# Optimization experiments

Measured on AMD Instinct MI355X. Metric: run time of the kernel, lower is better.

Reference implementation:

```python
import jax, jax.numpy as jnp
import numpy as np

N = 512            # input_size == number of graph nodes (X = I_N)
B = 64             # batch_size
H1, H2, H3 = 128, 64, 32   # hidden3 + 16 must equal 32 + class_nums
OUT = 8            # output_size; OUT*OUT + OUT == 72 (controller out channels)
CLS = 16           # class_nums (one-hot task encoding is 16-dim)


def setup_inputs():
    key = jax.random.key(0)
    ks = jax.random.split(key, 20)

    def u(k, shape, fan_out):
        s = 1.0 / np.sqrt(fan_out)
        return jax.random.uniform(k, shape, jnp.float32, -s, s)

    inp = {
        "adj": jax.random.uniform(ks[0], (B, 2, N, N), jnp.float32),
        "task_id": jax.random.randint(ks[1], (B,), 0, CLS),
    }
    dims = [(N, H1), (H1, H2), (H2, H3), (H3, OUT)]
    i = 2
    for pref in ("p", "n"):
        for l, (fi, fo) in enumerate(dims, 1):
            inp[f"w{l}{pref}"] = u(ks[i], (fi, fo), fo); i += 1
            inp[f"b{l}{pref}"] = u(ks[i], (fo,), fo); i += 1
    # controller: Conv1d(H3+CLS, 72, kernel=1, bias=False) -> stored as [72, H3+CLS]
    inp["wc"] = jax.random.normal(ks[i], (OUT * OUT + OUT, H3 + CLS), jnp.float32) * np.sqrt(2.0 / (OUT * OUT + OUT))
    return inp


def _normalize(adj):
    # D^-1/2 (A + I) D^-1/2, fully vectorized over [B, 2] (original loops in Python)
    a = adj + jnp.eye(adj.shape[-1], dtype=adj.dtype)
    d = a.sum(-1) ** -0.5                       # [B,2,N]
    return d[..., :, None] * a * d[..., None, :]


def _leaky(x):
    return jnp.where(x >= 0, x, 0.2 * x)


def _gcn_branch(feat, ws, bs):
    # feat: [B,N,N] normalized adjacency; X = I_N so first support = W1
    x = jnp.eye(N, dtype=feat.dtype)
    for i, (w, b) in enumerate(zip(ws, bs)):
        x = jnp.matmul(feat, jnp.matmul(x, w)) + b   # [B,N,fo]
        if i < len(ws) - 1:
            x = _leaky(x)
        if i == len(ws) - 2:
            conv3 = x
    return conv3, x                                  # ([B,N,H3], [B,N,OUT])


def _dcl(conv3, task_enc, conv4, wc):
    # conv3: [B,N,H3]; conv4: [B,N,OUT]; task_enc: [B,CLS]
    x_feat = conv3.mean(axis=1)                       # AdaptiveAvgPool1d over nodes -> [B,H3]
    x_cond = jnp.concatenate([x_feat, task_enc], 1)   # [B,H3+CLS]
    params = x_cond @ wc.T                            # [B,72]
    w = params[:, :OUT * OUT].reshape(B, OUT, OUT)    # per-sample dynamic head weights
    b = params[:, OUT * OUT:]                         # [B,OUT]
    # head_inputs = conv4.view(1,-1,N) with groups=B grouped conv1d (kernel 1)
    head = conv4.reshape(B, OUT, N)
    logits = jnp.einsum('boi,bin->bon', w, head) + b[..., None]   # [B,OUT,N]
    return logits.reshape(B, N, OUT)                  # faithful to torch reshape(N_,H_,-1)


def _forward(adj, task_id, w1p, b1p, w2p, b2p, w3p, b3p, w4p, b4p,
             w1n, b1n, w2n, b2n, w3n, b3n, w4n, b4n, wc):
    adj_n = _normalize(adj)
    feat_p, feat_n = adj_n[:, 0], adj_n[:, 1]
    p3, p4 = _gcn_branch(feat_p, [w1p, w2p, w3p, w4p], [b1p, b2p, b3p, b4p])
    n3, n4 = _gcn_branch(feat_n, [w1n, w2n, w3n, w4n], [b1n, b2n, b3n, b4n])
    te = jax.nn.one_hot(task_id, CLS, dtype=adj.dtype)   # encoding_task
    lp = _dcl(p3, te, p4, wc)
    ln = _dcl(n3, te, n4, wc)
    cc = jnp.concatenate([lp, ln], -1).reshape(-1, 2, N, OUT)  # [B,2,N,OUT]
    # F.dropout treated as identity (eval-mode determinism for reference)
    xm = jnp.matmul(cc, jnp.swapaxes(cc, -1, -2))              # [B,2,N,N]
    return jax.nn.log_sigmoid(xm) * -1.0


def reference(adj, task_id, w1p, b1p, w2p, b2p, w3p, b3p, w4p, b4p,
              w1n, b1n, w2n, b2n, w3n, b3n, w4n, b4n, wc):
    return _forward(adj, task_id, w1p, b1p, w2p, b2p, w3p, b3p, w4p, b4p,
                    w1n, b1n, w2n, b2n, w3n, b3n, w4n, b4n, wc)
```

## Files before the change

kernel.cpp:

```cpp
#include <hip/hip_runtime.h>
#include <math.h>

#define NN 512
#define NBC 128

__global__ __launch_bounds__(256) void k_rowsum(const float* __restrict__ adj,
                                                float* __restrict__ dinv) {
    int wave = blockIdx.x * 4 + (threadIdx.x >> 6);
    int lane = threadIdx.x & 63;
    const float4* row = (const float4*)(adj + (size_t)wave * NN);
    float4 v0 = row[lane], v1 = row[lane + 64];
    float s = v0.x + v0.y + v0.z + v0.w + v1.x + v1.y + v1.z + v1.w;
    #pragma unroll
    for (int off = 32; off; off >>= 1) s += __shfl_down(s, off, 64);
    if (lane == 0) dinv[wave] = rsqrtf(1.0f + s);
}

template<int H, int HP, bool SHARED, bool ACT>
__global__ __launch_bounds__(256) void k_biggemm(
    const float* __restrict__ adj, const float* __restrict__ zcg,
    const float* __restrict__ wp, const float* __restrict__ wn,
    const float* __restrict__ bp, const float* __restrict__ bn,
    const float* __restrict__ dinv, float* __restrict__ xout)
{
    constexpr int CPT = HP / 16;
    constexpr int KT = 64;
    __shared__ float a_s[64 * 68];
    __shared__ float z_s[KT * H];
    const int bc = blockIdx.y;
    const int rt = blockIdx.x;
    const int t  = threadIdx.x;
    const int tx = t & 15, ty = t >> 4;
    const float* A    = adj + (size_t)bc * NN * NN + (size_t)rt * 64 * NN;
    const float* dloc = dinv + bc * NN;
    const float* ZG   = SHARED ? ((bc & 1) ? wn : wp) : (zcg + (size_t)bc * NN * H);
    const float* bias = (bc & 1) ? bn : bp;

    float acc[4][CPT];
    #pragma unroll
    for (int r = 0; r < 4; ++r)
        #pragma unroll
        for (int u = 0; u < CPT; ++u) acc[r][u] = 0.f;

    for (int kb = 0; kb < NN; kb += KT) {
        __syncthreads();
        #pragma unroll
        for (int l = 0; l < 4; ++l) {
            int idx = t + l * 256;
            int r = idx >> 4, q = idx & 15;
            float4 v = *(const float4*)(A + (size_t)r * NN + kb + q * 4);
            *(float4*)(a_s + r * 68 + q * 4) = v;
        }
        constexpr int NZ4 = KT * H / 4;
        for (int idx = t; idx < NZ4; idx += 256) {
            int k = idx / (H / 4), hq = idx % (H / 4);
            float4 v = *(const float4*)(ZG + (size_t)(kb + k) * H + hq * 4);
            if (SHARED) {
                float dk = dloc[kb + k];
                v.x *= dk; v.y *= dk; v.z *= dk; v.w *= dk;
            }
            *(float4*)(z_s + k * H + hq * 4) = v;
        }
        __syncthreads();
        #pragma unroll 8
        for (int k = 0; k < KT; ++k) {
            float ar[4];
            #pragma unroll
            for (int r = 0; r < 4; ++r) ar[r] = a_s[(ty * 4 + r) * 68 + k];
            float zv[CPT];
            #pragma unroll
            for (int u = 0; u < CPT; ++u) {
                int h = tx * CPT + u;
                if (H < HP && h >= H) h = 0;
                zv[u] = z_s[k * H + h];
            }
            #pragma unroll
            for (int r = 0; r < 4; ++r)
                #pragma unroll
                for (int u = 0; u < CPT; ++u)
                    acc[r][u] += ar[r] * zv[u];
        }
    }
    #pragma unroll
    for (int r = 0; r < 4; ++r) {
        int i = rt * 64 + ty * 4 + r;
        float di = dloc[i];
        #pragma unroll
        for (int u = 0; u < CPT; ++u) {
            int h = tx * CPT + u;
            if (H < HP && h >= H) continue;
            float self = SHARED ? di * ZG[(size_t)i * H + h] : ZG[(size_t)i * H + h];
            float v = di * (acc[r][u] + self) + bias[h];
            if (ACT) v = v >= 0.f ? v : 0.2f * v;
            xout[((size_t)bc * NN + i) * H + h] = v;
        }
    }
}

template<int HI, int HO>
__global__ __launch_bounds__(256) void k_smallgemm(
    const float* __restrict__ xin, const float* __restrict__ wp,
    const float* __restrict__ wn, const float* __restrict__ dinv,
    float* __restrict__ zc)
{
    constexpr int CPT = (HO >= 16) ? HO / 16 : 1;
    constexpr int XS = HI + 4;
    __shared__ float x_s[32 * XS];
    __shared__ float w_s[HI * HO];
    const int bc = blockIdx.y, jt = blockIdx.x, t = threadIdx.x;
    const int tx = t & 15, ty = t >> 4;
    const float* W = (bc & 1) ? wn : wp;
    const float* X = xin + ((size_t)bc * NN + jt * 32) * HI;
    for (int idx = t; idx < HI * HO / 4; idx += 256)
        *(float4*)(w_s + idx * 4) = *(const float4*)(W + idx * 4);
    for (int idx = t; idx < 32 * HI / 4; idx += 256) {
        int r = idx / (HI / 4), q = idx % (HI / 4);
        *(float4*)(x_s + r * XS + q * 4) = *(const float4*)(X + (size_t)r * HI + q * 4);
    }
    __syncthreads();
    float acc[2][CPT];
    #pragma unroll
    for (int r = 0; r < 2; ++r)
        #pragma unroll
        for (int u = 0; u < CPT; ++u) acc[r][u] = 0.f;
    #pragma unroll 4
    for (int p = 0; p < HI; ++p) {
        float xr[2];
        #pragma unroll
        for (int r = 0; r < 2; ++r) xr[r] = x_s[(ty * 2 + r) * XS + p];
        float wv[CPT];
        #pragma unroll
        for (int u = 0; u < CPT; ++u) {
            int h = tx * CPT + u;
            if (HO < 16 && h >= HO) h = 0;
            wv[u] = w_s[p * HO + h];
        }
        #pragma unroll
        for (int r = 0; r < 2; ++r)
            #pragma unroll
            for (int u = 0; u < CPT; ++u) acc[r][u] += xr[r] * wv[u];
    }
    const float* dloc = dinv + bc * NN;
    #pragma unroll
    for (int r = 0; r < 2; ++r) {
        int j = jt * 32 + ty * 2 + r;
        float dj = dloc[j];
        #pragma unroll
        for (int u = 0; u < CPT; ++u) {
            int h = tx * CPT + u;
            if (HO < 16 && h >= HO) continue;
            zc[((size_t)bc * NN + j) * HO + h] = dj * acc[r][u];
        }
    }
}

__global__ __launch_bounds__(256) void k_dcl(
    const float* __restrict__ x3, const float* __restrict__ x4,
    const float* __restrict__ wc, const int* __restrict__ task,
    float* __restrict__ L)
{
    __shared__ float ps[8][32];
    __shared__ float xf[32];
    __shared__ float pr[72];
    const int bc = blockIdx.x, t = threadIdx.x;
    const float* X3 = x3 + (size_t)bc * NN * 32;
    {
        int col = t & 31, rg = t >> 5;
        float s = 0.f;
        for (int r = rg; r < NN; r += 8) s += X3[r * 32 + col];
        ps[rg][col] = s;
    }
    __syncthreads();
    if (t < 32) {
        float s = 0.f;
        #pragma unroll
        for (int g = 0; g < 8; ++g) s += ps[g][t];
        xf[t] = s * (1.0f / 512.0f);
    }
    __syncthreads();
    if (t < 72) {
        int tid = task[bc >> 1];
        const float* wr = wc + t * 48;
        float s = wr[32 + tid];
        #pragma unroll
        for (int j = 0; j < 32; ++j) s += wr[j] * xf[j];
        pr[t] = s;
    }
    __syncthreads();
    const float* X4 = x4 + (size_t)bc * 4096;
    float* Lb = L + (size_t)bc * 4096;
    #pragma unroll
    for (int rep = 0; rep < 2; ++rep) {
        int n = rep * 256 + t;
        float hi[8];
        #pragma unroll
        for (int i = 0; i < 8; ++i) hi[i] = X4[i * 512 + n];
        #pragma unroll
        for (int o = 0; o < 8; ++o) {
            float s = pr[64 + o];
            #pragma unroll
            for (int i = 0; i < 8; ++i) s += pr[o * 8 + i] * hi[i];
            Lb[o * 512 + n] = s;
        }
    }
}

#define SCP 520
__global__ __launch_bounds__(256) void k_final(const float* __restrict__ L,
                                               float* __restrict__ out)
{
    __shared__ float scT[8 * SCP];
    const int bcid = blockIdx.y;
    const int b = bcid >> 1, c = bcid & 1;
    const int nt = blockIdx.x, t = threadIdx.x;
    const float* Lp = L + (size_t)(b * 2) * 4096;
    const float* Ln = Lp + 4096;
    for (int rep = 0; rep < 16; ++rep) {
        int e = rep * 256 + t;
        int f = c * 4096 + e;
        int n = f >> 4, k = f & 15;
        float v = (k < 8) ? Lp[n * 8 + k] : Ln[n * 8 + k - 8];
        scT[(e & 7) * SCP + (e >> 3)] = v;
    }
    __syncthreads();
    const int tx = t & 63, ty = t >> 6;
    const int n0 = nt * 32 + ty * 8;
    float cn[8][8];
    #pragma unroll
    for (int o = 0; o < 8; ++o)
        #pragma unroll
        for (int i = 0; i < 8; ++i) cn[i][o] = scT[o * SCP + n0 + i];
    float* ob = out + (size_t)bcid * NN * NN;
    #pragma unroll 2
    for (int mg = 0; mg < 8; ++mg) {
        int m = tx + mg * 64;
        float cm[8];
        #pragma unroll
        for (int o = 0; o < 8; ++o) cm[o] = scT[o * SCP + m];
        #pragma unroll
        for (int i = 0; i < 8; ++i) {
            float s = 0.f;
            #pragma unroll
            for (int o = 0; o < 8; ++o) s += cn[i][o] * cm[o];
            float r = fmaxf(-s, 0.f) + __logf(1.0f + __expf(-fabsf(s)));
            ob[(size_t)(n0 + i) * NN + m] = r;
        }
    }
}

extern "C" void kernel_launch(void* const* d_in, const int* in_sizes, int n_in,
                              void* d_out, int out_size, void* d_ws, size_t ws_size,
                              hipStream_t stream)
{
    const float* adj = (const float*)d_in[0];
    const int*  task = (const int*)d_in[1];
    const float* w1p = (const float*)d_in[2];  const float* b1p = (const float*)d_in[3];
    const float* w2p = (const float*)d_in[4];  const float* b2p = (const float*)d_in[5];
    const float* w3p = (const float*)d_in[6];  const float* b3p = (const float*)d_in[7];
    const float* w4p = (const float*)d_in[8];  const float* b4p = (const float*)d_in[9];
    const float* w1n = (const float*)d_in[10]; const float* b1n = (const float*)d_in[11];
    const float* w2n = (const float*)d_in[12]; const float* b2n = (const float*)d_in[13];
    const float* w3n = (const float*)d_in[14]; const float* b3n = (const float*)d_in[15];
    const float* w4n = (const float*)d_in[16]; const float* b4n = (const float*)d_in[17];
    const float* wc  = (const float*)d_in[18];

    float* ws   = (float*)d_ws;
    float* dinv = ws;
    float* XA   = ws + 65536;
    float* X3   = XA + 8388608;
    float* X4   = X3 + 2097152;
    float* L    = X4 + 524288;
    float* ZC   = L  + 524288;
    (void)in_sizes; (void)n_in; (void)out_size; (void)ws_size;

    k_rowsum<<<dim3(NBC * NN / 4), dim3(256), 0, stream>>>(adj, dinv);
    k_biggemm<128,128,true ,true ><<<dim3(8,128), 256, 0, stream>>>(adj, nullptr, w1p, w1n, b1p, b1n, dinv, XA);
    k_smallgemm<128,64><<<dim3(16,128), 256, 0, stream>>>(XA, w2p, w2n, dinv, ZC);
    k_biggemm<64,64,false,true ><<<dim3(8,128), 256, 0, stream>>>(adj, ZC, nullptr, nullptr, b2p, b2n, dinv, XA);
    k_smallgemm<64,32><<<dim3(16,128), 256, 0, stream>>>(XA, w3p, w3n, dinv, ZC);
    k_biggemm<32,32,false,true ><<<dim3(8,128), 256, 0, stream>>>(adj, ZC, nullptr, nullptr, b3p, b3n, dinv, X3);
    k_smallgemm<32,8><<<dim3(16,128), 256, 0, stream>>>(X3, w4p, w4n, dinv, ZC);
    k_biggemm<8,16,false,false><<<dim3(8,128), 256, 0, stream>>>(adj, ZC, nullptr, nullptr, b4p, b4n, dinv, X4);
    k_dcl<<<dim3(128), 256, 0, stream>>>(X3, X4, wc, task, L);
    k_final<<<dim3(16,128), 256, 0, stream>>>(L, (float*)d_out);
}
```

Measured before the change: 617.0 us.

## Use split-bf16 MFMA GEMMs with a pre-normalized bf16 adjacency copy

Adds a path that normalizes the adjacency once and stores it as hi/lo bf16 pairs. All GCN GEMMs then run on MFMA 16x16x32 bf16 instructions, using three products per tile to keep close to fp32 accuracy. Weights are pre-transposed and split, and intermediate activations are written in split-bf16 form for the next layer. This trades extra memory traffic (a 128 MB adjacency copy plus conversion passes) and a ~198 MB workspace requirement for much higher matrix throughput than the scalar fp32 FMA kernels. The old path is kept as a fallback when the workspace is too small.

```diff
diff --git a/kernel.cpp b/kernel.cpp
--- a/kernel.cpp
+++ b/kernel.cpp
@@ -3,6 +3,19 @@
 
 #define NN 512
 #define NBC 128
+
+typedef __attribute__((ext_vector_type(8))) __bf16 v8bf;
+typedef __attribute__((ext_vector_type(4))) float v4f;
+
+__device__ __forceinline__ void bsplit(float v, unsigned short& h, unsigned short& l) {
+    unsigned u  = __builtin_bit_cast(unsigned, v);
+    unsigned hb = (u + 0x7fffu + ((u >> 16) & 1u)) & 0xffff0000u;
+    float hf    = __builtin_bit_cast(float, hb);
+    h = (unsigned short)(hb >> 16);
+    float lof   = v - hf;
+    unsigned ul = __builtin_bit_cast(unsigned, lof);
+    l = (unsigned short)((ul + 0x7fffu + ((ul >> 16) & 1u)) >> 16);
+}
 
 __global__ __launch_bounds__(256) void k_rowsum(const float* __restrict__ adj,
                                                 float* __restrict__ dinv) {
@@ -14,6 +27,153 @@
     #pragma unroll
     for (int off = 32; off; off >>= 1) s += __shfl_down(s, off, 64);
     if (lane == 0) dinv[wave] = rsqrtf(1.0f + s);
+}
+
+__global__ __launch_bounds__(256) void k_convert(const float* __restrict__ adj,
+    const float* __restrict__ dinv, unsigned short* __restrict__ anh,
+    unsigned short* __restrict__ anl)
+{
+    unsigned gid = blockIdx.x * 256 + threadIdx.x;
+    unsigned e = gid * 4;
+    unsigned bc = e >> 18, rem = e & 0x3ffffu;
+    unsigned i = rem >> 9, j = rem & 511u;
+    float4 a = *(const float4*)(adj + (size_t)e);
+    float di = dinv[bc * NN + i];
+    const float4 dj = *(const float4*)(dinv + bc * NN + j);
+    float v0 = di * dj.x * (a.x + ((j + 0) == i ? 1.f : 0.f));
+    float v1 = di * dj.y * (a.y + ((j + 1) == i ? 1.f : 0.f));
+    float v2 = di * dj.z * (a.z + ((j + 2) == i ? 1.f : 0.f));
+    float v3 = di * dj.w * (a.w + ((j + 3) == i ? 1.f : 0.f));
+    ushort4 hh, ll;
+    bsplit(v0, hh.x, ll.x); bsplit(v1, hh.y, ll.y);
+    bsplit(v2, hh.z, ll.z); bsplit(v3, hh.w, ll.w);
+    *(ushort4*)(anh + e) = hh;
+    *(ushort4*)(anl + e) = ll;
+}
+
+struct WJob  { const float* w; unsigned short* dh; unsigned short* dl; int HI; int HO; int HOP; };
+struct WJobs { WJob j[8]; };
+__global__ __launch_bounds__(256) void k_wprep(WJobs jobs) {
+    WJob jb = jobs.j[blockIdx.y];
+    int idx = blockIdx.x * 256 + threadIdx.x;
+    if (idx >= jb.HOP * jb.HI) return;
+    int h = idx / jb.HI, p = idx % jb.HI;
+    float v = (h < jb.HO) ? jb.w[p * jb.HO + h] : 0.f;
+    unsigned short hh, ll; bsplit(v, hh, ll);
+    jb.dh[idx] = hh; jb.dl[idx] = ll;
+}
+
+template<int BN, int OUTW, bool SHAREDZ, bool ACT, bool WBF>
+__global__ __launch_bounds__(256, 2) void k_mfma(
+    const unsigned short* __restrict__ anh_, const unsigned short* __restrict__ anl_,
+    const unsigned short* __restrict__ zh_,  const unsigned short* __restrict__ zl_,
+    const float* __restrict__ bp, const float* __restrict__ bn,
+    float* __restrict__ xf, unsigned short* __restrict__ xh, unsigned short* __restrict__ xl)
+{
+    constexpr int C = BN / 16;
+    const int bc = blockIdx.y, rb = blockIdx.x;
+    const int t = threadIdx.x, w = t >> 6, lane = t & 63;
+    const int m0 = lane & 15, quad = lane >> 4;
+    const int rowbase = rb * 128 + w * 32;
+    const int s = SHAREDZ ? (bc & 1) : bc;
+    const unsigned short* pa_h = anh_ + ((size_t)bc * NN + rowbase + m0) * NN + quad * 8;
+    const unsigned short* pa_l = anl_ + ((size_t)bc * NN + rowbase + m0) * NN + quad * 8;
+    const unsigned short* pz_h = zh_ + ((size_t)s * BN + m0) * NN + quad * 8;
+    const unsigned short* pz_l = zl_ + ((size_t)s * BN + m0) * NN + quad * 8;
+    v4f acc[2][C];
+    #pragma unroll
+    for (int r = 0; r < 2; ++r)
+        #pragma unroll
+        for (int c = 0; c < C; ++c) acc[r][c] = (v4f){0.f, 0.f, 0.f, 0.f};
+
+    for (int kb = 0; kb < 16; ++kb) {
+        const int ko = kb * 32;
+        v8bf zfh[C], zfl[C];
+        #pragma unroll
+        for (int c = 0; c < C; ++c) {
+            zfh[c] = *(const v8bf*)(pz_h + (size_t)(c * 16) * NN + ko);
+            zfl[c] = *(const v8bf*)(pz_l + (size_t)(c * 16) * NN + ko);
+        }
+        #pragma unroll
+        for (int r = 0; r < 2; ++r) {
+            v8bf ah = *(const v8bf*)(pa_h + (size_t)(r * 16) * NN + ko);
+            v8bf al = *(const v8bf*)(pa_l + (size_t)(r * 16) * NN + ko);
+            #pragma unroll
+            for (int c = 0; c < C; ++c) {
+                acc[r][c] = __builtin_amdgcn_mfma_f32_16x16x32_bf16(ah, zfh[c], acc[r][c], 0, 0, 0);
+                acc[r][c] = __builtin_amdgcn_mfma_f32_16x16x32_bf16(ah, zfl[c], acc[r][c], 0, 0, 0);
+                acc[r][c] = __builtin_amdgcn_mfma_f32_16x16x32_bf16(al, zfh[c], acc[r][c], 0, 0, 0);
+            }
+        }
+    }
+    const float* bias = (bc & 1) ? bn : bp;
+    #pragma unroll
+    for (int r = 0; r < 2; ++r)
+        #pragma unroll
+        for (int c = 0; c < C; ++c) {
+            int col = c * 16 + m0;
+            if (OUTW < BN && col >= OUTW) continue;
+            float bv = bias[col];
+            #pragma unroll
+            for (int reg = 0; reg < 4; ++reg) {
+                int row = rowbase + r * 16 + quad * 4 + reg;
+                float v = acc[r][c][reg] + bv;
+                if (ACT) v = v >= 0.f ? v : 0.2f * v;
+                size_t oi = ((size_t)bc * NN + row) * OUTW + col;
+                if (xf) xf[oi] = v;
+                if (WBF) {
+                    unsigned short hh, ll; bsplit(v, hh, ll);
+                    xh[oi] = hh; xl[oi] = ll;
+                }
+            }
+        }
+}
+
+template<int HI, int HOP>
+__global__ __launch_bounds__(256) void k_zgemm(
+    const unsigned short* __restrict__ wth, const unsigned short* __restrict__ wtl,
+    const unsigned short* __restrict__ xh_, const unsigned short* __restrict__ xl_,
+    unsigned short* __restrict__ zh_, unsigned short* __restrict__ zl_)
+{
+    constexpr int MT = HOP / 16, JW = 4 / MT, NT = 8 / JW;
+    const int bc = blockIdx.y, jb = blockIdx.x;
+    const int t = threadIdx.x, w = t >> 6, lane = t & 63;
+    const int m0 = lane & 15, quad = lane >> 4;
+    const int mt = w % MT, jseg = w / MT;
+    const int n0 = jb * 128 + jseg * (128 / JW);
+    const int s = bc & 1;
+    const unsigned short* pw_h = wth + ((size_t)s * HOP + mt * 16 + m0) * HI + quad * 8;
+    const unsigned short* pw_l = wtl + ((size_t)s * HOP + mt * 16 + m0) * HI + quad * 8;
+    const unsigned short* px_h = xh_ + ((size_t)bc * NN + n0 + m0) * HI + quad * 8;
+    const unsigned short* px_l = xl_ + ((size_t)bc * NN + n0 + m0) * HI + quad * 8;
+    v4f acc[NT];
+    #pragma unroll
+    for (int c = 0; c < NT; ++c) acc[c] = (v4f){0.f, 0.f, 0.f, 0.f};
+    #pragma unroll
+    for (int ks = 0; ks < HI / 32; ++ks) {
+        const int ko = ks * 32;
+        v8bf awh = *(const v8bf*)(pw_h + ko);
+        v8bf awl = *(const v8bf*)(pw_l + ko);
+        #pragma unroll
+        for (int c = 0; c < NT; ++c) {
+            v8bf bxh = *(const v8bf*)(px_h + (size_t)(c * 16) * HI + ko);
+            v8bf bxl = *(const v8bf*)(px_l + (size_t)(c * 16) * HI + ko);
+            acc[c] = __builtin_amdgcn_mfma_f32_16x16x32_bf16(awh, bxh, acc[c], 0, 0, 0);
+            acc[c] = __builtin_amdgcn_mfma_f32_16x16x32_bf16(awh, bxl, acc[c], 0, 0, 0);
+            acc[c] = __builtin_amdgcn_mfma_f32_16x16x32_bf16(awl, bxh, acc[c], 0, 0, 0);
+        }
+    }
+    #pragma unroll
+    for (int c = 0; c < NT; ++c) {
+        int j = n0 + c * 16 + m0;
+        #pragma unroll
+        for (int reg = 0; reg < 4; ++reg) {
+            int h = mt * 16 + quad * 4 + reg;
+            unsigned short hh, ll; bsplit(acc[c][reg], hh, ll);
+            size_t oi = ((size_t)bc * HOP + h) * NN + j;
+            zh_[oi] = hh; zl_[oi] = ll;
+        }
+    }
 }
 
 template<int H, int HP, bool SHARED, bool ACT>
@@ -35,13 +195,11 @@
     const float* dloc = dinv + bc * NN;
     const float* ZG   = SHARED ? ((bc & 1) ? wn : wp) : (zcg + (size_t)bc * NN * H);
     const float* bias = (bc & 1) ? bn : bp;
-
     float acc[4][CPT];
     #pragma unroll
     for (int r = 0; r < 4; ++r)
         #pragma unroll
         for (int u = 0; u < CPT; ++u) acc[r][u] = 0.f;
-
     for (int kb = 0; kb < NN; kb += KT) {
         __syncthreads();
         #pragma unroll
@@ -263,24 +421,77 @@
     const float* w3n = (const float*)d_in[14]; const float* b3n = (const float*)d_in[15];
     const float* w4n = (const float*)d_in[16]; const float* b4n = (const float*)d_in[17];
     const float* wc  = (const float*)d_in[18];
-
-    float* ws   = (float*)d_ws;
-    float* dinv = ws;
-    float* XA   = ws + 65536;
-    float* X3   = XA + 8388608;
-    float* X4   = X3 + 2097152;
-    float* L    = X4 + 524288;
-    float* ZC   = L  + 524288;
-    (void)in_sizes; (void)n_in; (void)out_size; (void)ws_size;
-
-    k_rowsum<<<dim3(NBC * NN / 4), dim3(256), 0, stream>>>(adj, dinv);
-    k_biggemm<128,128,true ,true ><<<dim3(8,128), 256, 0, stream>>>(adj, nullptr, w1p, w1n, b1p, b1n, dinv, XA);
-    k_smallgemm<128,64><<<dim3(16,128), 256, 0, stream>>>(XA, w2p, w2n, dinv, ZC);
-    k_biggemm<64,64,false,true ><<<dim3(8,128), 256, 0, stream>>>(adj, ZC, nullptr, nullptr, b2p, b2n, dinv, XA);
-    k_smallgemm<64,32><<<dim3(16,128), 256, 0, stream>>>(XA, w3p, w3n, dinv, ZC);
-    k_biggemm<32,32,false,true ><<<dim3(8,128), 256, 0, stream>>>(adj, ZC, nullptr, nullptr, b3p, b3n, dinv, X3);
-    k_smallgemm<32,8><<<dim3(16,128), 256, 0, stream>>>(X3, w4p, w4n, dinv, ZC);
-    k_biggemm<8,16,false,false><<<dim3(8,128), 256, 0, stream>>>(adj, ZC, nullptr, nullptr, b4p, b4n, dinv, X4);
-    k_dcl<<<dim3(128), 256, 0, stream>>>(X3, X4, wc, task, L);
-    k_final<<<dim3(16,128), 256, 0, stream>>>(L, (float*)d_out);
-}
+    (void)in_sizes; (void)n_in; (void)out_size;
+
+    const size_t NEED = 198004736ull;
+    if (ws_size >= NEED) {
+        char* base = (char*)d_ws;
+        float*          dinv = (float*)(base + 0);
+        unsigned short* anh  = (unsigned short*)(base + 262144);
+        unsigned short* anl  = (unsigned short*)(base + 67371008);
+        unsigned short* zt1h = (unsigned short*)(base + 134479872);
+        unsigned short* zt1l = (unsigned short*)(base + 134742016);
+        unsigned short* wt2h = (unsigned short*)(base + 135004160);
+        unsigned short* wt2l = (unsigned short*)(base + 135036928);
+        unsigned short* wt3h = (unsigned short*)(base + 135069696);
+        unsigned short* wt3l = (unsigned short*)(base + 135077888);
+        unsigned short* wt4h = (unsigned short*)(base + 135086080);
+        unsigned short* wt4l = (unsigned short*)(base + 135088128);
+        unsigned short* x1h  = (unsigned short*)(base + 135090176);
+        unsigned short* x1l  = (unsigned short*)(base + 151867392);
+        unsigned short* zt2h = (unsigned short*)(base + 168644608);
+        unsigned short* zt2l = (unsigned short*)(base + 177033216);
+        float*          x3f  = (float*)(base + 185421824);
+        float*          x4f  = (float*)(base + 193810432);
+        float*          L    = (float*)(base + 195907584);
+        unsigned short* x2h = x1h,  *x2l = x1l;
+        unsigned short* x3h = x1h,  *x3l = x1l;
+        unsigned short* zt3h = zt2h, *zt3l = zt2l;
+        unsigned short* zt4h = zt2h, *zt4l = zt2l;
+
+        k_rowsum<<<dim3(NBC * NN / 4), 256, 0, stream>>>(adj, dinv);
+        k_convert<<<dim3(32768), 256, 0, stream>>>(adj, dinv, anh, anl);
+        WJobs jobs;
+        jobs.j[0] = {w1p, zt1h,          zt1l,          512, 128, 128};
+        jobs.j[1] = {w1n, zt1h + 65536,  zt1l + 65536,  512, 128, 128};
+        jobs.j[2] = {w2p, wt2h,          wt2l,          128,  64,  64};
+        jobs.j[3] = {w2n, wt2h + 8192,   wt2l + 8192,   128,  64,  64};
+        jobs.j[4] = {w3p, wt3h,          wt3l,           64,  32,  32};
+        jobs.j[5] = {w3n, wt3h + 2048,   wt3l + 2048,    64,  32,  32};
+        jobs.j[6] = {w4p, wt4h,          wt4l,           32,   8,  16};
+        jobs.j[7] = {w4n, wt4h + 512,    wt4l + 512,     32,   8,  16};
+        k_wprep<<<dim3(256, 8), 256, 0, stream>>>(jobs);
+
+        k_mfma<128, 128, true,  true,  true ><<<dim3(4, NBC), 256, 0, stream>>>(
+            anh, anl, zt1h, zt1l, b1p, b1n, nullptr, x1h, x1l);
+        k_zgemm<128, 64><<<dim3(4, NBC), 256, 0, stream>>>(wt2h, wt2l, x1h, x1l, zt2h, zt2l);
+        k_mfma<64, 64, false, true,  true ><<<dim3(4, NBC), 256, 0, stream>>>(
+            anh, anl, zt2h, zt2l, b2p, b2n, nullptr, x2h, x2l);
+        k_zgemm<64, 32><<<dim3(4, NBC), 256, 0, stream>>>(wt3h, wt3l, x2h, x2l, zt3h, zt3l);
+        k_mfma<32, 32, false, true,  true ><<<dim3(4, NBC), 256, 0, stream>>>(
+            anh, anl, zt3h, zt3l, b3p, b3n, x3f, x3h, x3l);
+        k_zgemm<32, 16><<<dim3(4, NBC), 256, 0, stream>>>(wt4h, wt4l, x3h, x3l, zt4h, zt4l);
+        k_mfma<16, 8, false, false, false><<<dim3(4, NBC), 256, 0, stream>>>(
+            anh, anl, zt4h, zt4l, b4p, b4n, x4f, nullptr, nullptr);
+        k_dcl<<<dim3(NBC), 256, 0, stream>>>(x3f, x4f, wc, task, L);
+        k_final<<<dim3(16, NBC), 256, 0, stream>>>(L, (float*)d_out);
+    } else {
+        float* ws   = (float*)d_ws;
+        float* dinv = ws;
+        float* XA   = ws + 65536;
+        float* X3   = XA + 8388608;
+        float* X4   = X3 + 2097152;
+        float* L    = X4 + 524288;
+        float* ZC   = L  + 524288;
+        k_rowsum<<<dim3(NBC * NN / 4), 256, 0, stream>>>(adj, dinv);
+        k_biggemm<128,128,true ,true ><<<dim3(8,128), 256, 0, stream>>>(adj, nullptr, w1p, w1n, b1p, b1n, dinv, XA);
+        k_smallgemm<128,64><<<dim3(16,128), 256, 0, stream>>>(XA, w2p, w2n, dinv, ZC);
+        k_biggemm<64,64,false,true ><<<dim3(8,128), 256, 0, stream>>>(adj, ZC, nullptr, nullptr, b2p, b2n, dinv, XA);
+        k_smallgemm<64,32><<<dim3(16,128), 256, 0, stream>>>(XA, w3p, w3n, dinv, ZC);
+        k_biggemm<32,32,false,true ><<<dim3(8,128), 256, 0, stream>>>(adj, ZC, nullptr, nullptr, b3p, b3n, dinv, X3);
+        k_smallgemm<32,8><<<dim3(16,128), 256, 0, stream>>>(X3, w4p, w4n, dinv, ZC);
+        k_biggemm<8,16,false,false><<<dim3(8,128), 256, 0, stream>>>(adj, ZC, nullptr, nullptr, b4p, b4n, dinv, X4);
+        k_dcl<<<dim3(128), 256, 0, stream>>>(X3, X4, wc, task, L);
+        k_final<<<dim3(16,128), 256, 0, stream>>>(L, (float*)d_out);
+    }
+}
```

Measured after the change: 572.3 us. -7.3%, faster.
